# Optimization experiments

Measured on AMD Instinct MI355X. Metric: run time of the kernel, lower is better.

The kernel has to match this reference:

```python
import jax, jax.numpy as jnp
import numpy as np
import math

D = 256; H = 8; L = 6; DK = D // H

def _ln(x, g, b):
    m = jnp.mean(x, -1, keepdims=True)
    v = jnp.mean((x - m) ** 2, -1, keepdims=True)
    return (x - m) * jax.lax.rsqrt(v + 1e-5) * g + b

def setup_inputs() -> dict:
    key = jax.random.key(0)
    ks = jax.random.split(key, 16)
    B, N, F, E = 8, 768, 128, 4
    s = 0.02
    inp = {}
    inp['node_feats'] = jax.random.normal(ks[0], (B, N, F), jnp.float32)
    inp['adj'] = jax.random.randint(ks[1], (B, N, N), 0, 2, jnp.int32)
    inp['dist'] = jax.random.uniform(ks[2], (B, N, N), jnp.float32)
    inp['edge_type_oh'] = jax.random.uniform(ks[3], (B, N, N, E), jnp.float32)
    inp['node_proj_w'] = jax.random.normal(ks[4], (F, D), jnp.float32) * s
    inp['node_proj_b'] = jnp.zeros((D,), jnp.float32)
    inp['cls'] = jax.random.normal(ks[5], (1, 1, D), jnp.float32) * s
    inp['etw'] = jax.random.normal(ks[6], (E,), jnp.float32) * s
    inp['noedge_bias'] = jnp.float32(-2.0)
    inp['deg_scale'] = jnp.float32(0.2)
    inp['gamma'] = jnp.float32(0.8)
    inp['v2n'] = jnp.float32(0.1)
    inp['n2v'] = jnp.float32(0.1)
    inp['vself'] = jnp.float32(0.05)
    inp['ln1_g'] = jnp.ones((L, D), jnp.float32); inp['ln1_b'] = jnp.zeros((L, D), jnp.float32)
    inp['qw'] = jax.random.normal(ks[7], (L, D, D), jnp.float32) * s; inp['qb'] = jnp.zeros((L, D), jnp.float32)
    inp['kw'] = jax.random.normal(ks[8], (L, D, D), jnp.float32) * s; inp['kb'] = jnp.zeros((L, D), jnp.float32)
    inp['vw'] = jax.random.normal(ks[9], (L, D, D), jnp.float32) * s; inp['vb'] = jnp.zeros((L, D), jnp.float32)
    inp['ow'] = jax.random.normal(ks[10], (L, D, D), jnp.float32) * s; inp['ob'] = jnp.zeros((L, D), jnp.float32)
    inp['ln2_g'] = jnp.ones((L, D), jnp.float32); inp['ln2_b'] = jnp.zeros((L, D), jnp.float32)
    Dm = int(D * 1.0)  # mlp_ratio=1.0
    inp['fc1w'] = jax.random.normal(ks[11], (L, D, Dm), jnp.float32) * s; inp['fc1b'] = jnp.zeros((L, Dm), jnp.float32)
    inp['fc2w'] = jax.random.normal(ks[12], (L, Dm, D), jnp.float32) * s; inp['fc2b'] = jnp.zeros((L, D), jnp.float32)
    return inp

def _build_bias(adj_f, dist, edge_type_oh, etw, noedge_bias, deg_scale, gamma, v2n, n2v, vself):
    # DynamicAttnBiasBuilder: hard_mask=False, use_degree=True, vnode_spd_mode='replace', gamma != 0
    B, N, _ = adj_f.shape
    T = N + 1
    e = jnp.einsum('bije,e->bij', edge_type_oh, etw) - gamma * dist  # (B,N,N)
    e = jnp.where(adj_f > 0, e, e + noedge_bias)
    deg = adj_f.sum(-1)  # (B,N)
    deg_norm = (deg[:, :, None] + deg[:, None, :]) / (deg.max(axis=1, keepdims=True)[:, :, None] + 1e-6)
    e = e + deg_scale * deg_norm
    bias = jnp.zeros((B, T, T), jnp.float32)
    bias = bias.at[:, 1:, 1:].set(e)
    bias = bias.at[:, 0, 1:].set(v2n)   # vnode_spd_mode == 'replace'
    bias = bias.at[:, 1:, 0].set(n2v)
    bias = bias.at[:, 0, 0].set(vself)
    return bias  # (B,T,T), broadcast over heads

def _mhsa(x, bias, qw, qb, kw, kb, vw, vb, ow, ob):
    B, T, _ = x.shape
    q = (x @ qw + qb).reshape(B, T, H, DK).transpose(0, 2, 1, 3)
    k = (x @ kw + kb).reshape(B, T, H, DK).transpose(0, 2, 1, 3)
    v = (x @ vw + vb).reshape(B, T, H, DK).transpose(0, 2, 1, 3)
    scores = jnp.einsum('bhqd,bhkd->bhqk', q, k) / math.sqrt(DK)
    scores = scores + bias[:, None, :, :]
    attn = jax.nn.softmax(scores, axis=-1)
    out = jnp.einsum('bhqk,bhkd->bhqd', attn, v)
    out = out.transpose(0, 2, 1, 3).reshape(B, T, D)
    return out @ ow + ob

def _forward(node_feats, adj, dist, edge_type_oh, node_proj_w, node_proj_b, cls,
             etw, noedge_bias, deg_scale, gamma, v2n, n2v, vself,
             ln1_g, ln1_b, qw, qb, kw, kb, vw, vb, ow, ob,
             ln2_g, ln2_b, fc1w, fc1b, fc2w, fc2b):
    adj_f = adj.astype(jnp.float32)
    bias = _build_bias(adj_f, dist, edge_type_oh, etw, noedge_bias, deg_scale, gamma, v2n, n2v, vself)
    B = node_feats.shape[0]
    x = node_feats @ node_proj_w + node_proj_b  # (B,N,D)
    x = jnp.concatenate([jnp.broadcast_to(cls, (B, 1, D)), x], axis=1)  # prepend virtual node -> (B,T,D)
    for l in range(L):
        h = _mhsa(_ln(x, ln1_g[l], ln1_b[l]), bias, qw[l], qb[l], kw[l], kb[l], vw[l], vb[l], ow[l], ob[l])
        x = x + h
        m = _ln(x, ln2_g[l], ln2_b[l])
        m = jax.nn.gelu(m @ fc1w[l] + fc1b[l], approximate=False) @ fc2w[l] + fc2b[l]
        x = x + m
    return x

def reference(node_feats, adj, dist, edge_type_oh, node_proj_w, node_proj_b, cls,
              etw, noedge_bias, deg_scale, gamma, v2n, n2v, vself,
              ln1_g, ln1_b, qw, qb, kw, kb, vw, vb, ow, ob,
              ln2_g, ln2_b, fc1w, fc1b, fc2w, fc2b):
    return _forward(node_feats, adj, dist, edge_type_oh, node_proj_w, node_proj_b, cls,
                    etw, noedge_bias, deg_scale, gamma, v2n, n2v, vself,
                    ln1_g, ln1_b, qw, qb, kw, kb, vw, vb, ow, ob,
                    ln2_g, ln2_b, fc1w, fc1b, fc2w, fc2b)
```

## Files before the change

### kernel.cpp

```cpp
#include <hip/hip_runtime.h>
#include <math.h>

#define BB 8
#define NN 768
#define TT 769
#define DD 256
#define HH 8
#define DKK 32
#define FF 128
#define LL 6
#define MM 6152
#define SCALE 0.17677669529663687f
#define TP 832
#define KQP 784
#define KHS (KQP * DKK)
#define GBP 776
#define HP 264
#define WSZ 65536

typedef __attribute__((ext_vector_type(8))) short s16x8;
typedef __attribute__((ext_vector_type(8))) unsigned short u16x8;
typedef __attribute__((ext_vector_type(4))) float f32x4;

__device__ inline short f2bf(float x) {
    unsigned u = __float_as_uint(x);
    unsigned r = (u + 0x7FFFu + ((u >> 16) & 1u)) >> 16;
    return (short)r;
}
__device__ inline float bf2f(unsigned short s) {
    return __uint_as_float(((unsigned)s) << 16);
}
__device__ inline float gelu_f(float x) {
    return 0.5f * x * (1.f + erff(x * 0.70710678118654752f));
}

__global__ __launch_bounds__(256) void deg_kernel(const int* __restrict__ adj,
                                                  float* __restrict__ deg) {
    int row  = blockIdx.x * 4 + (threadIdx.x >> 6);
    int lane = threadIdx.x & 63;
    const int* p = adj + (size_t)row * NN;
    int s = 0;
#pragma unroll
    for (int i = 0; i < NN / 64; ++i) s += p[lane + 64 * i];
#pragma unroll
    for (int off = 32; off > 0; off >>= 1) s += __shfl_xor(s, off);
    if (lane == 0) deg[row] = (float)s;
}

__global__ __launch_bounds__(256) void degmax_kernel(const float* __restrict__ deg,
                                                     float* __restrict__ dmax) {
    __shared__ float red[256];
    int b = blockIdx.x, t = threadIdx.x;
    float m = 0.f;
    for (int i = t; i < NN; i += 256) m = fmaxf(m, deg[b * NN + i]);
    red[t] = m;
    __syncthreads();
    for (int s = 128; s > 0; s >>= 1) {
        if (t < s) red[t] = fmaxf(red[t], red[t + s]);
        __syncthreads();
    }
    if (t == 0) dmax[b] = red[0];
}

__global__ __launch_bounds__(256) void bias_kernel(
    const float* __restrict__ dist, const float* __restrict__ eoh,
    const int* __restrict__ adj, const float* __restrict__ deg,
    const float* __restrict__ dmax, const float* __restrict__ etw,
    const float* __restrict__ noedge, const float* __restrict__ degsc,
    const float* __restrict__ gamma, const float* __restrict__ v2n,
    const float* __restrict__ n2v, const float* __restrict__ vself,
    unsigned short* __restrict__ bias)
{
    long long idx = (long long)blockIdx.x * 256 + threadIdx.x;
    const long long total = (long long)BB * TT * GBP;
    if (idx >= total) return;
    int b  = (int)(idx / ((long long)TT * GBP));
    int r  = (int)(idx % ((long long)TT * GBP));
    int qi = r / GBP, kj = r % GBP;
    float out;
    if (kj >= TT)                out = 0.f;
    else if (qi == 0 && kj == 0) out = vself[0];
    else if (qi == 0)            out = v2n[0];
    else if (kj == 0)            out = n2v[0];
    else {
        int i = qi - 1, j = kj - 1;
        size_t e = ((size_t)b * NN + i) * NN + j;
        float4 oh = *(const float4*)(eoh + 4 * e);
        float val = oh.x * etw[0] + oh.y * etw[1] + oh.z * etw[2] + oh.w * etw[3]
                    - gamma[0] * dist[e];
        if (adj[e] == 0) val += noedge[0];
        val += degsc[0] * (deg[b * NN + i] + deg[b * NN + j]) / (dmax[b] + 1e-6f);
        out = val;
    }
    bias[idx] = (unsigned short)f2bf(out);
}

__global__ __launch_bounds__(256) void nodeproj_ln_kernel(
    const float* __restrict__ nf, const float* __restrict__ w,
    const float* __restrict__ bsv, const float* __restrict__ cls,
    const float* __restrict__ g, const float* __restrict__ bvec,
    float* __restrict__ x, short* __restrict__ xn)
{
    __shared__ float sf[FF];
    __shared__ float red[256];
    int row = blockIdx.x, t = threadIdx.x;
    int b = row / TT, tr = row % TT;
    float y;
    if (tr == 0) {
        y = cls[t];
    } else {
        if (t < FF) sf[t] = nf[((size_t)b * NN + tr - 1) * FF + t];
        __syncthreads();
        y = bsv[t];
#pragma unroll 8
        for (int kk = 0; kk < FF; ++kk) y = fmaf(sf[kk], w[kk * DD + t], y);
    }
    x[(size_t)row * DD + t] = y;
    red[t] = y;
    __syncthreads();
    for (int s = 128; s > 0; s >>= 1) { if (t < s) red[t] += red[t + s]; __syncthreads(); }
    float mean = red[0] * (1.f / DD);
    __syncthreads();
    float d = y - mean;
    red[t] = d * d;
    __syncthreads();
    for (int s = 128; s > 0; s >>= 1) { if (t < s) red[t] += red[t + s]; __syncthreads(); }
    float var = red[0] * (1.f / DD);
    xn[(size_t)row * DD + t] = f2bf(d * rsqrtf(var + 1e-5f) * g[t] + bvec[t]);
}

__global__ __launch_bounds__(256) void wtrans_kernel(
    const float* __restrict__ qw, const float* __restrict__ kw,
    const float* __restrict__ vw, const float* __restrict__ ow,
    const float* __restrict__ f1w, const float* __restrict__ f2w,
    short* __restrict__ wt2)
{
    int mi = blockIdx.x >> 4, kg = blockIdx.x & 15;
    int fam = mi / 6, l = mi % 6;
    const float* W;
    if      (fam == 0) W = qw;
    else if (fam == 1) W = kw;
    else if (fam == 2) W = vw;
    else if (fam == 3) W = ow;
    else if (fam == 4) W = f1w;
    else               W = f2w;
    W += (size_t)l * DD * DD;
    int n = threadIdx.x;
    short* out = wt2 + (size_t)mi * WSZ;
#pragma unroll
    for (int kk = 0; kk < 16; ++kk) {
        int k = kg * 16 + kk;
        float val = W[(size_t)k * DD + n];
        size_t idx = (size_t)(((n >> 4) * 8 + (k >> 5)) * 512
                   + (((k >> 3) & 3) * 16 + (n & 15)) * 8 + (k & 7));
        out[idx] = f2bf(val);
    }
}

__global__ __launch_bounds__(256) void gemm_qkv_kernel(
    const short* __restrict__ A, const short* __restrict__ wtl,
    const float* __restrict__ qb, const float* __restrict__ kb,
    const float* __restrict__ vb,
    short* __restrict__ qh, short* __restrict__ kh, short* __restrict__ vtb)
{
    int t = threadIdx.x;
    int w = t >> 6, lane = t & 63, quad = lane >> 4, m16 = lane & 15;
    int m0 = blockIdx.x * 16;
    int fam = blockIdx.y;
    const short* Wf = wtl + (size_t)fam * 6 * WSZ;
    const float* bsv = fam == 0 ? qb : (fam == 1 ? kb : vb);
    int arow = m0 + m16; if (arow >= MM) arow = MM - 1;
    const short* ap = A + (size_t)arow * DD + quad * 8;
    const short* wbase = Wf + (size_t)(w * 4) * 4096 + lane * 8;
    f32x4 acc[4] = {};
#pragma unroll
    for (int kc = 0; kc < 8; ++kc) {
        s16x8 af = *(const s16x8*)(ap + kc * 32);
#pragma unroll
        for (int nt = 0; nt < 4; ++nt) {
            s16x8 bf = *(const s16x8*)(wbase + (size_t)nt * 4096 + kc * 512);
            acc[nt] = __builtin_amdgcn_mfma_f32_16x16x32_bf16(af, bf, acc[nt], 0, 0, 0);
        }
    }
    if (fam < 2) {
        short* outp = fam == 0 ? qh : kh;
#pragma unroll
        for (int r = 0; r < 4; ++r) {
            int row = m0 + quad * 4 + r;
            if (row < MM) {
                int b = row / TT;
                int tpos = row - b * TT;
                size_t rb = ((size_t)b * HH * KQP + tpos) * DKK;
#pragma unroll
                for (int nt = 0; nt < 4; ++nt) {
                    int col = w * 64 + nt * 16 + m16;
                    float bv = bsv[col];
                    int h = col >> 5, dk = col & 31;
                    outp[rb + (size_t)h * KHS + dk] = f2bf(acc[nt][r] + bv);
                }
            }
        }
    } else {
#pragma unroll
        for (int nt = 0; nt < 4; ++nt) {
            int col = w * 64 + nt * 16 + m16;
            float bv = bsv[col];
            int h = col >> 5, dk = col & 31;
#pragma unroll
            for (int r = 0; r < 4; ++r) {
                int row = m0 + quad * 4 + r;
                if (row < MM) {
                    int b = row / TT;
                    int tpos = row - b * TT;
                    vtb[(((size_t)(b * HH + h)) * DKK + dk) * TP + tpos] =
                        f2bf(acc[nt][r] + bv);
                }
            }
        }
    }
}

__global__ __launch_bounds__(512) void mega_kernel(
    const short* __restrict__ q, const short* __restrict__ k,
    const short* __restrict__ vt, const unsigned short* __restrict__ bias,
    const short* __restrict__ Wo, const short* __restrict__ W1,
    const short* __restrict__ W2,
    const float* __restrict__ ob, const float* __restrict__ g2,
    const float* __restrict__ b2, const float* __restrict__ f1b,
    const float* __restrict__ f2b, float* __restrict__ x,
    short* __restrict__ xn, const float* __restrict__ g1,
    const float* __restrict__ b1, int donext)
{
    __shared__ short Pb[8][16][72];
    __shared__ short xa[16][HP];
    __shared__ short xnl[16][HP];
    __shared__ short hb[16][HP];
    __shared__ float redS[16][8], redQ[16][8];

    int t = threadIdx.x;
    int w = t >> 6, lane = t & 63;
    int quad = lane >> 4, m16 = lane & 15;
    int bx = blockIdx.x;
    int b = bx / 49;
    int qt = bx - b * 49;
    int h = w;
    int q0 = qt * 16;

    size_t rb4[4];
#pragma unroll
    for (int r = 0; r < 4; ++r) {
        int qr = q0 + quad * 4 + r; if (qr >= TT) qr = TT - 1;
        rb4[r] = (size_t)(b * TT + qr) * GBP;
    }

    int qrow = q0 + m16;
    int qc = qrow < TT ? qrow : TT - 1;
    const short* qbase = q + (size_t)(b * HH + h) * KHS;
    s16x8 qa = *(const s16x8*)(qbase + (size_t)qc * DKK + quad * 8);

    const short* kbase = k + (size_t)(b * HH + h) * KHS;
    const short* vbase = vt + (((size_t)(b * HH + h)) * DKK) * TP;

    s16x8 kfA[4], kfB[4], vfA[4], vfB[4];
    unsigned short bbA[16], bbB[16];
    f32x4 sacc[4];
    f32x4 o0 = {0.f, 0.f, 0.f, 0.f};
    f32x4 o1 = {0.f, 0.f, 0.f, 0.f};
    float ls[4] = {0.f, 0.f, 0.f, 0.f};

#define LOADK_(DST, CC)                                                         \
    {                                                                           \
        _Pragma("unroll") for (int s = 0; s < 4; ++s) {                         \
            int kr = (CC) * 64 + s * 16 + m16;                                  \
            int kcl = kr < TT ? kr : TT - 1;                                    \
            DST[s] = *(const s16x8*)(kbase + (size_t)kcl * DKK + quad * 8);     \
        }                                                                       \
    }
#define LOADV_(DST, CC)                                                         \
    {                                                                           \
        int jn = (CC) * 64;                                                     \
        DST[0] = *(const s16x8*)(vbase + (size_t)m16 * TP + jn + quad * 8);     \
        DST[1] = *(const s16x8*)(vbase + (size_t)m16 * TP + jn + 32 + quad * 8);\
        DST[2] = *(const s16x8*)(vbase + (size_t)(16 + m16) * TP + jn + quad * 8);\
        DST[3] = *(const s16x8*)(vbase + (size_t)(16 + m16) * TP + jn + 32 + quad * 8);\
    }
#define LOADB_(DST, CC)                                                         \
    {                                                                           \
        _Pragma("unroll") for (int s = 0; s < 4; ++s) {                         \
            int ko = (CC) * 64 + s * 16 + m16;                                  \
            ko = ko < TT ? ko : 0;                                              \
            _Pragma("unroll") for (int r = 0; r < 4; ++r)                       \
                DST[s * 4 + r] = bias[rb4[r] + ko];                             \
        }                                                                       \
    }
#define STEP_(C, KPRE, KUSE, VUSE, VPRE, BUSE, BPRE, DOPREK, DOPREV, DOPREB, DOQK) \
    {                                                                           \
        if (DOPREK) LOADK_(KPRE, (C) + 2);                                      \
        if (DOPREV) LOADV_(VPRE, (C) + 1);                                      \
        if (DOPREB) LOADB_(BPRE, (C) + 1);                                      \
        int j0 = (C) * 64;                                                      \
        _Pragma("unroll") for (int s = 0; s < 4; ++s) {                         \
            int key = j0 + s * 16 + m16;                                        \
            int kv = key < TT;                                                  \
            _Pragma("unroll") for (int r = 0; r < 4; ++r) {                     \
                float bv = bf2f(BUSE[s * 4 + r]);                               \
                float sval = kv ? fmaf(sacc[s][r], SCALE, bv) : -1e30f;         \
                float p = __expf(sval - 8.0f);                                  \
                ls[r] += p;                                                     \
                Pb[w][quad * 4 + r][s * 16 + m16] = f2bf(p);                    \
            }                                                                   \
        }                                                                       \
        if (DOQK) {                                                             \
            f32x4 z = {0.f, 0.f, 0.f, 0.f};                                     \
            _Pragma("unroll") for (int s = 0; s < 4; ++s)                       \
                sacc[s] = __builtin_amdgcn_mfma_f32_16x16x32_bf16(qa, KUSE[s], z, 0, 0, 0); \
        }                                                                       \
        s16x8 pa0 = *(const s16x8*)&Pb[w][m16][quad * 8];                       \
        s16x8 pa1 = *(const s16x8*)&Pb[w][m16][32 + quad * 8];                  \
        o0 = __builtin_amdgcn_mfma_f32_16x16x32_bf16(pa0, VUSE[0], o0, 0, 0, 0);\
        o0 = __builtin_amdgcn_mfma_f32_16x16x32_bf16(pa1, VUSE[1], o0, 0, 0, 0);\
        o1 = __builtin_amdgcn_mfma_f32_16x16x32_bf16(pa0, VUSE[2], o1, 0, 0, 0);\
        o1 = __builtin_amdgcn_mfma_f32_16x16x32_bf16(pa1, VUSE[3], o1, 0, 0, 0);\
    }

    LOADK_(kfA, 0);
    LOADK_(kfB, 1);
    LOADV_(vfA, 0);
    LOADB_(bbA, 0);
    {
        f32x4 z = {0.f, 0.f, 0.f, 0.f};
#pragma unroll
        for (int s = 0; s < 4; ++s)
            sacc[s] = __builtin_amdgcn_mfma_f32_16x16x32_bf16(qa, kfA[s], z, 0, 0, 0);
    }
    for (int cc = 0; cc < 5; ++cc) {
        STEP_(2 * cc,     kfA, kfB, vfA, vfB, bbA, bbB, 1, 1, 1, 1)
        STEP_(2 * cc + 1, kfB, kfA, vfB, vfA, bbB, bbA, 1, 1, 1, 1)
    }
    STEP_(10, kfA, kfB, vfA, vfB, bbA, bbB, 1, 1, 1, 1)
    STEP_(11, kfB, kfA, vfB, vfA, bbB, bbA, 0, 1, 1, 1)
    STEP_(12, kfA, kfB, vfA, vfB, bbA, bbB, 0, 0, 0, 0)

#undef STEP_
#undef LOADB_
#undef LOADV_
#undef LOADK_

#pragma unroll
    for (int r = 0; r < 4; ++r) {
        float l = ls[r];
#pragma unroll
        for (int off = 1; off < 16; off <<= 1) l += __shfl_xor(l, off);
        float inv = 1.f / l;
        int rl = quad * 4 + r;
        xa[rl][h * DKK + m16]      = f2bf(o0[r] * inv);
        xa[rl][h * DKK + 16 + m16] = f2bf(o1[r] * inv);
    }
    __syncthreads();

    const short* wob = Wo + (size_t)(w * 2) * 4096 + lane * 8;
    f32x4 acco[2] = {};
#pragma unroll
    for (int kc = 0; kc < 8; ++kc) {
        s16x8 af = *(const s16x8*)&xa[m16][kc * 32 + quad * 8];
#pragma unroll
        for (int ntl = 0; ntl < 2; ++ntl) {
            s16x8 bf = *(const s16x8*)(wob + (size_t)ntl * 4096 + kc * 512);
            acco[ntl] = __builtin_amdgcn_mfma_f32_16x16x32_bf16(af, bf, acco[ntl], 0, 0, 0);
        }
    }
    float vv[2][4], sr[4], q2[4];
#pragma unroll
    for (int r = 0; r < 4; ++r) { sr[r] = 0.f; q2[r] = 0.f; }
#pragma unroll
    for (int ntl = 0; ntl < 2; ++ntl) {
        int col = w * 32 + ntl * 16 + m16;
        float bv = ob[col];
#pragma unroll
        for (int r = 0; r < 4; ++r) {
            int row = q0 + quad * 4 + r; if (row >= TT) row = TT - 1;
            float v = acco[ntl][r] + bv + x[((size_t)(b * TT + row)) * DD + col];
            vv[ntl][r] = v; sr[r] += v; q2[r] += v * v;
        }
    }
#pragma unroll
    for (int r = 0; r < 4; ++r)
#pragma unroll
        for (int off = 1; off < 16; off <<= 1) {
            sr[r] += __shfl_xor(sr[r], off);
            q2[r] += __shfl_xor(q2[r], off);
        }
    if (m16 == 0) {
#pragma unroll
        for (int r = 0; r < 4; ++r) {
            redS[quad * 4 + r][w] = sr[r];
            redQ[quad * 4 + r][w] = q2[r];
        }
    }
    __syncthreads();

#pragma unroll
    for (int r = 0; r < 4; ++r) {
        int rl = quad * 4 + r;
        float fs = 0.f, fq = 0.f;
#pragma unroll
        for (int j = 0; j < 8; ++j) { fs += redS[rl][j]; fq += redQ[rl][j]; }
        float mean = fs * (1.f / DD);
        float var = fq * (1.f / DD) - mean * mean;
        float inv = rsqrtf(var + 1e-5f);
#pragma unroll
        for (int ntl = 0; ntl < 2; ++ntl) {
            int col = w * 32 + ntl * 16 + m16;
            xnl[rl][col] = f2bf((vv[ntl][r] - mean) * inv * g2[col] + b2[col]);
        }
    }
    __syncthreads();

    const short* w1b = W1 + (size_t)(w * 2) * 4096 + lane * 8;
    f32x4 acc1[2] = {};
#pragma unroll
    for (int kc = 0; kc < 8; ++kc) {
        s16x8 af = *(const s16x8*)&xnl[m16][kc * 32 + quad * 8];
#pragma unroll
        for (int ntl = 0; ntl < 2; ++ntl) {
            s16x8 bf = *(const s16x8*)(w1b + (size_t)ntl * 4096 + kc * 512);
            acc1[ntl] = __builtin_amdgcn_mfma_f32_16x16x32_bf16(af, bf, acc1[ntl], 0, 0, 0);
        }
    }
#pragma unroll
    for (int ntl = 0; ntl < 2; ++ntl) {
        int col = w * 32 + ntl * 16 + m16;
        float fb = f1b[col];
#pragma unroll
        for (int r = 0; r < 4; ++r)
            hb[quad * 4 + r][col] = f2bf(gelu_f(acc1[ntl][r] + fb));
    }
    __syncthreads();

    const short* w2b = W2 + (size_t)(w * 2) * 4096 + lane * 8;
    f32x4 acc2[2] = {};
#pragma unroll
    for (int kc = 0; kc < 8; ++kc) {
        s16x8 af = *(const s16x8*)&hb[m16][kc * 32 + quad * 8];
#pragma unroll
        for (int ntl = 0; ntl < 2; ++ntl) {
            s16x8 bf = *(const s16x8*)(w2b + (size_t)ntl * 4096 + kc * 512);
            acc2[ntl] = __builtin_amdgcn_mfma_f32_16x16x32_bf16(af, bf, acc2[ntl], 0, 0, 0);
        }
    }
#pragma unroll
    for (int r = 0; r < 4; ++r) { sr[r] = 0.f; q2[r] = 0.f; }
#pragma unroll
    for (int ntl = 0; ntl < 2; ++ntl) {
        int col = w * 32 + ntl * 16 + m16;
        float bv = f2b[col];
#pragma unroll
        for (int r = 0; r < 4; ++r) {
            float v = acc2[ntl][r] + bv + vv[ntl][r];
            vv[ntl][r] = v; sr[r] += v; q2[r] += v * v;
        }
    }
#pragma unroll
    for (int r = 0; r < 4; ++r)
#pragma unroll
        for (int off = 1; off < 16; off <<= 1) {
            sr[r] += __shfl_xor(sr[r], off);
            q2[r] += __shfl_xor(q2[r], off);
        }
    if (m16 == 0) {
#pragma unroll
        for (int r = 0; r < 4; ++r) {
            redS[quad * 4 + r][w] = sr[r];
            redQ[quad * 4 + r][w] = q2[r];
        }
    }
    __syncthreads();

#pragma unroll
    for (int r = 0; r < 4; ++r) {
        int rl = quad * 4 + r;
        int row = q0 + rl;
        float fs = 0.f, fq = 0.f;
#pragma unroll
        for (int j = 0; j < 8; ++j) { fs += redS[rl][j]; fq += redQ[rl][j]; }
        float mean = fs * (1.f / DD);
        float var = fq * (1.f / DD) - mean * mean;
        float inv = rsqrtf(var + 1e-5f);
        if (row < TT) {
            size_t grow = (size_t)(b * TT + row) * DD;
#pragma unroll
            for (int ntl = 0; ntl < 2; ++ntl) {
                int col = w * 32 + ntl * 16 + m16;
                float v = vv[ntl][r];
                x[grow + col] = v;
                if (donext)
                    xn[grow + col] = f2bf((v - mean) * inv * g1[col] + b1[col]);
            }
        }
    }
}

extern "C" void kernel_launch(void* const* d_in, const int* in_sizes, int n_in,
                              void* d_out, int out_size, void* d_ws, size_t ws_size,
                              hipStream_t stream)
{
    const float* node_feats = (const float*)d_in[0];
    const int*   adj        = (const int*)d_in[1];
    const float* dist       = (const float*)d_in[2];
    const float* eoh        = (const float*)d_in[3];
    const float* npw        = (const float*)d_in[4];
    const float* npb        = (const float*)d_in[5];
    const float* cls        = (const float*)d_in[6];
    const float* etw        = (const float*)d_in[7];
    const float* noedge     = (const float*)d_in[8];
    const float* degsc      = (const float*)d_in[9];
    const float* gamma      = (const float*)d_in[10];
    const float* v2n        = (const float*)d_in[11];
    const float* n2v        = (const float*)d_in[12];
    const float* vself      = (const float*)d_in[13];
    const float* ln1g = (const float*)d_in[14];
    const float* ln1b = (const float*)d_in[15];
    const float* qw   = (const float*)d_in[16];
    const float* qb   = (const float*)d_in[17];
    const float* kw   = (const float*)d_in[18];
    const float* kb   = (const float*)d_in[19];
    const float* vw   = (const float*)d_in[20];
    const float* vb   = (const float*)d_in[21];
    const float* ow   = (const float*)d_in[22];
    const float* ob   = (const float*)d_in[23];
    const float* ln2g = (const float*)d_in[24];
    const float* ln2b = (const float*)d_in[25];
    const float* f1w  = (const float*)d_in[26];
    const float* f1b  = (const float*)d_in[27];
    const float* f2w  = (const float*)d_in[28];
    const float* f2b  = (const float*)d_in[29];

    float* x  = (float*)d_out;
    char* ws = (char*)d_ws;
    size_t off = 0;
    unsigned short* bias = (unsigned short*)(ws + off); off += (size_t)BB * TT * GBP * 2;
    float* deg  = (float*)(ws + off); off += (size_t)BB * NN * 4;
    float* dmax = (float*)(ws + off); off += 64;
    short* xn16 = (short*)(ws + off); off += (size_t)MM * DD * 2;
    short* qhb  = (short*)(ws + off); off += (size_t)BB * HH * KQP * DKK * 2;
    short* khb  = (short*)(ws + off); off += (size_t)BB * HH * KQP * DKK * 2;
    short* vtb  = (short*)(ws + off); off += (size_t)BB * HH * DKK * TP * 2;
    short* wt2  = (short*)(ws + off); off += (size_t)36 * WSZ * 2;

    deg_kernel<<<(BB * NN) / 4, 256, 0, stream>>>(adj, deg);
    degmax_kernel<<<BB, 256, 0, stream>>>(deg, dmax);

    long long total = (long long)BB * TT * GBP;
    bias_kernel<<<(int)((total + 255) / 256), 256, 0, stream>>>(
        dist, eoh, adj, deg, dmax, etw, noedge, degsc, gamma, v2n, n2v, vself, bias);

    nodeproj_ln_kernel<<<MM, 256, 0, stream>>>(node_feats, npw, npb, cls,
                                               ln1g, ln1b, x, xn16);

    wtrans_kernel<<<576, 256, 0, stream>>>(qw, kw, vw, ow, f1w, f2w, wt2);

    dim3 gqkv(385, 3);
    for (int l = 0; l < LL; ++l) {
        size_t bo = (size_t)l * DD;
        gemm_qkv_kernel<<<gqkv, 256, 0, stream>>>(xn16, wt2 + (size_t)l * WSZ,
                                                  qb + bo, kb + bo, vb + bo,
                                                  qhb, khb, vtb);
        int donext = (l + 1 < LL) ? 1 : 0;
        size_t bn = (size_t)(l + 1 < LL ? l + 1 : 0) * DD;
        mega_kernel<<<392, 512, 0, stream>>>(
            qhb, khb, vtb, bias,
            wt2 + (size_t)(3 * 6 + l) * WSZ,
            wt2 + (size_t)(4 * 6 + l) * WSZ,
            wt2 + (size_t)(5 * 6 + l) * WSZ,
            ob + bo, ln2g + bo, ln2b + bo, f1b + bo, f2b + bo,
            x, xn16, ln1g + bn, ln1b + bn, donext);
    }
}
```

Before: 730.7 us.

## Prepack attention bias into per-lane fragment layout and deepen V prefetch

Adds a one-time kernel that rearranges the bf16 attention bias into the exact per-lane order the MFMA score fragments consume. Each lane in the attention loop then does two 16-byte vector loads per chunk instead of sixteen scattered 2-byte gathers. The V prefetch is also deepened from one chunk ahead to two, using a third register buffer. The cost is an extra pre-pass kernel, a second bias-sized workspace buffer, and more live registers in the mega kernel.

```diff
diff --git a/kernel.cpp b/kernel.cpp
--- a/kernel.cpp
+++ b/kernel.cpp
@@ -17,6 +17,7 @@
 #define GBP 776
 #define HP 264
 #define WSZ 65536
+#define NPK ((size_t)BB * 49 * 13 * 1024)
 
 typedef __attribute__((ext_vector_type(8))) short s16x8;
 typedef __attribute__((ext_vector_type(8))) unsigned short u16x8;
@@ -95,6 +96,23 @@
     bias[idx] = (unsigned short)f2bf(out);
 }
 
+__global__ __launch_bounds__(256) void biaspk_kernel(
+    const unsigned short* __restrict__ bias, unsigned short* __restrict__ bpk)
+{
+    int idx = blockIdx.x * 256 + threadIdx.x;
+    int jj   = idx & 7;
+    int lane = (idx >> 3) & 63;
+    int half = (idx >> 9) & 1;
+    int c    = (idx >> 10) % 13;
+    int qtb  = idx / (13 * 1024);
+    int b = qtb / 49, qt = qtb - b * 49;
+    int quad = lane >> 4, m16 = lane & 15;
+    int j = half * 8 + jj, s = j >> 2, r = j & 3;
+    int kj = c * 64 + s * 16 + m16; if (kj >= TT) kj = 0;
+    int qi = qt * 16 + quad * 4 + r; if (qi >= TT) qi = TT - 1;
+    bpk[idx] = bias[(size_t)(b * TT + qi) * GBP + kj];
+}
+
 __global__ __launch_bounds__(256) void nodeproj_ln_kernel(
     const float* __restrict__ nf, const float* __restrict__ w,
     const float* __restrict__ bsv, const float* __restrict__ cls,
@@ -222,7 +240,7 @@
 
 __global__ __launch_bounds__(512) void mega_kernel(
     const short* __restrict__ q, const short* __restrict__ k,
-    const short* __restrict__ vt, const unsigned short* __restrict__ bias,
+    const short* __restrict__ vt, const unsigned short* __restrict__ bpk,
     const short* __restrict__ Wo, const short* __restrict__ W1,
     const short* __restrict__ W2,
     const float* __restrict__ ob, const float* __restrict__ g2,
@@ -245,13 +263,7 @@
     int qt = bx - b * 49;
     int h = w;
     int q0 = qt * 16;
-
-    size_t rb4[4];
-#pragma unroll
-    for (int r = 0; r < 4; ++r) {
-        int qr = q0 + quad * 4 + r; if (qr >= TT) qr = TT - 1;
-        rb4[r] = (size_t)(b * TT + qr) * GBP;
-    }
+    size_t qtb13 = (size_t)(b * 49 + qt) * 13;
 
     int qrow = q0 + m16;
     int qc = qrow < TT ? qrow : TT - 1;
@@ -261,8 +273,8 @@
     const short* kbase = k + (size_t)(b * HH + h) * KHS;
     const short* vbase = vt + (((size_t)(b * HH + h)) * DKK) * TP;
 
-    s16x8 kfA[4], kfB[4], vfA[4], vfB[4];
-    unsigned short bbA[16], bbB[16];
+    s16x8 kfA[4], kfB[4], vfA[4], vfB[4], vfC[4];
+    u16x8 bbA0, bbA1, bbB0, bbB1;
     f32x4 sacc[4];
     f32x4 o0 = {0.f, 0.f, 0.f, 0.f};
     f32x4 o1 = {0.f, 0.f, 0.f, 0.f};
@@ -284,26 +296,25 @@
         DST[2] = *(const s16x8*)(vbase + (size_t)(16 + m16) * TP + jn + quad * 8);\
         DST[3] = *(const s16x8*)(vbase + (size_t)(16 + m16) * TP + jn + 32 + quad * 8);\
     }
-#define LOADB_(DST, CC)                                                         \
+#define LOADB_(D0, D1, CC)                                                      \
     {                                                                           \
-        _Pragma("unroll") for (int s = 0; s < 4; ++s) {                         \
-            int ko = (CC) * 64 + s * 16 + m16;                                  \
-            ko = ko < TT ? ko : 0;                                              \
-            _Pragma("unroll") for (int r = 0; r < 4; ++r)                       \
-                DST[s * 4 + r] = bias[rb4[r] + ko];                             \
-        }                                                                       \
-    }
-#define STEP_(C, KPRE, KUSE, VUSE, VPRE, BUSE, BPRE, DOPREK, DOPREV, DOPREB, DOQK) \
+        const unsigned short* bp_ = bpk + ((qtb13 + (CC)) << 10);               \
+        D0 = *(const u16x8*)(bp_ + (lane << 3));                                \
+        D1 = *(const u16x8*)(bp_ + 512 + (lane << 3));                          \
+    }
+#define STEP_(C, KPRE, KUSE, VUSE, VPRE, BU0, BU1, BP0, BP1, PK, PV, PBF, DOQK) \
     {                                                                           \
-        if (DOPREK) LOADK_(KPRE, (C) + 2);                                      \
-        if (DOPREV) LOADV_(VPRE, (C) + 1);                                      \
-        if (DOPREB) LOADB_(BPRE, (C) + 1);                                      \
+        if (PK)  LOADK_(KPRE, (C) + 2);                                         \
+        if (PV)  LOADV_(VPRE, (C) + 2);                                         \
+        if (PBF) LOADB_(BP0, BP1, (C) + 1);                                     \
         int j0 = (C) * 64;                                                      \
         _Pragma("unroll") for (int s = 0; s < 4; ++s) {                         \
             int key = j0 + s * 16 + m16;                                        \
             int kv = key < TT;                                                  \
             _Pragma("unroll") for (int r = 0; r < 4; ++r) {                     \
-                float bv = bf2f(BUSE[s * 4 + r]);                               \
+                int j = s * 4 + r;                                              \
+                float bv = bf2f(j < 8 ? (unsigned short)BU0[j]                  \
+                                      : (unsigned short)BU1[j - 8]);            \
                 float sval = kv ? fmaf(sacc[s][r], SCALE, bv) : -1e30f;         \
                 float p = __expf(sval - 8.0f);                                  \
                 ls[r] += p;                                                     \
@@ -326,20 +337,28 @@
     LOADK_(kfA, 0);
     LOADK_(kfB, 1);
     LOADV_(vfA, 0);
-    LOADB_(bbA, 0);
+    LOADV_(vfB, 1);
+    LOADB_(bbA0, bbA1, 0);
     {
         f32x4 z = {0.f, 0.f, 0.f, 0.f};
 #pragma unroll
         for (int s = 0; s < 4; ++s)
             sacc[s] = __builtin_amdgcn_mfma_f32_16x16x32_bf16(qa, kfA[s], z, 0, 0, 0);
     }
-    for (int cc = 0; cc < 5; ++cc) {
-        STEP_(2 * cc,     kfA, kfB, vfA, vfB, bbA, bbB, 1, 1, 1, 1)
-        STEP_(2 * cc + 1, kfB, kfA, vfB, vfA, bbB, bbA, 1, 1, 1, 1)
-    }
-    STEP_(10, kfA, kfB, vfA, vfB, bbA, bbB, 1, 1, 1, 1)
-    STEP_(11, kfB, kfA, vfB, vfA, bbB, bbA, 0, 1, 1, 1)
-    STEP_(12, kfA, kfB, vfA, vfB, bbA, bbB, 0, 0, 0, 0)
+
+    STEP_(0,  kfA, kfB, vfA, vfC, bbA0, bbA1, bbB0, bbB1, 1, 1, 1, 1)
+    STEP_(1,  kfB, kfA, vfB, vfA, bbB0, bbB1, bbA0, bbA1, 1, 1, 1, 1)
+    STEP_(2,  kfA, kfB, vfC, vfB, bbA0, bbA1, bbB0, bbB1, 1, 1, 1, 1)
+    STEP_(3,  kfB, kfA, vfA, vfC, bbB0, bbB1, bbA0, bbA1, 1, 1, 1, 1)
+    STEP_(4,  kfA, kfB, vfB, vfA, bbA0, bbA1, bbB0, bbB1, 1, 1, 1, 1)
+    STEP_(5,  kfB, kfA, vfC, vfB, bbB0, bbB1, bbA0, bbA1, 1, 1, 1, 1)
+    STEP_(6,  kfA, kfB, vfA, vfC, bbA0, bbA1, bbB0, bbB1, 1, 1, 1, 1)
+    STEP_(7,  kfB, kfA, vfB, vfA, bbB0, bbB1, bbA0, bbA1, 1, 1, 1, 1)
+    STEP_(8,  kfA, kfB, vfC, vfB, bbA0, bbA1, bbB0, bbB1, 1, 1, 1, 1)
+    STEP_(9,  kfB, kfA, vfA, vfC, bbB0, bbB1, bbA0, bbA1, 1, 1, 1, 1)
+    STEP_(10, kfA, kfB, vfB, vfA, bbA0, bbA1, bbB0, bbB1, 1, 1, 1, 1)
+    STEP_(11, kfB, kfA, vfC, vfB, bbB0, bbB1, bbA0, bbA1, 0, 0, 1, 1)
+    STEP_(12, kfA, kfB, vfA, vfC, bbA0, bbA1, bbB0, bbB1, 0, 0, 0, 0)
 
 #undef STEP_
 #undef LOADB_
@@ -539,6 +558,7 @@
     char* ws = (char*)d_ws;
     size_t off = 0;
     unsigned short* bias = (unsigned short*)(ws + off); off += (size_t)BB * TT * GBP * 2;
+    unsigned short* bpk  = (unsigned short*)(ws + off); off += NPK * 2;
     float* deg  = (float*)(ws + off); off += (size_t)BB * NN * 4;
     float* dmax = (float*)(ws + off); off += 64;
     short* xn16 = (short*)(ws + off); off += (size_t)MM * DD * 2;
@@ -553,6 +573,8 @@
     long long total = (long long)BB * TT * GBP;
     bias_kernel<<<(int)((total + 255) / 256), 256, 0, stream>>>(
         dist, eoh, adj, deg, dmax, etw, noedge, degsc, gamma, v2n, n2v, vself, bias);
+
+    biaspk_kernel<<<(int)(NPK / 256), 256, 0, stream>>>(bias, bpk);
 
     nodeproj_ln_kernel<<<MM, 256, 0, stream>>>(node_feats, npw, npb, cls,
                                                ln1g, ln1b, x, xn16);
@@ -568,7 +590,7 @@
         int donext = (l + 1 < LL) ? 1 : 0;
         size_t bn = (size_t)(l + 1 < LL ? l + 1 : 0) * DD;
         mega_kernel<<<392, 512, 0, stream>>>(
-            qhb, khb, vtb, bias,
+            qhb, khb, vtb, bpk,
             wt2 + (size_t)(3 * 6 + l) * WSZ,
             wt2 + (size_t)(4 * 6 + l) * WSZ,
             wt2 + (size_t)(5 * 6 + l) * WSZ,
```

Measured after the change: 729.3 us. About the same (-0.2%).
